# Performance work log

Measured on AMD Instinct MI355X. Metric: run time of the kernel, lower is better.

Reference implementation:

```python
import jax, jax.numpy as jnp
import numpy as np

B, S, D = 2, 1024, 1024
E, K, F, FS = 8, 2, 512, 1024

def setup_inputs() -> dict:
    key = jax.random.key(0)
    ks = jax.random.split(key, 9)
    s = lambda k, shape, fan: jax.random.normal(k, shape, jnp.float32) * (fan ** -0.5)
    return {
        "x": jax.random.normal(ks[0], (B, S, D), jnp.float32),
        "Wr": s(ks[1], (D, E), D),
        "Wg": s(ks[2], (E, D, F), D),
        "Wu": s(ks[3], (E, D, F), D),
        "Wd": s(ks[4], (E, F, D), F),
        "Sg": s(ks[5], (D, FS), D),
        "Su": s(ks[6], (D, FS), D),
        "Sd": s(ks[7], (FS, D), FS),
        "expert_bias": jnp.zeros((E,), jnp.float32),
    }

def reference(x, Wr, Wg, Wu, Wd, Sg, Su, Sd, expert_bias):
    b, s, d = x.shape
    xf = x.reshape(-1, d)                              # [T, D]
    T = xf.shape[0]
    logits = xf @ Wr + expert_bias                     # [T, E]
    top_v, top_i = jax.lax.top_k(logits, K)            # [T, K]
    probs = jax.nn.softmax(top_v, axis=-1)             # [T, K]
    # dense routing-weight matrix: zero for non-selected experts
    rw = jnp.zeros_like(logits).at[jnp.arange(T)[:, None], top_i].set(probs)  # [T, E]
    # SwiGLU experts, computed densely; routing weight zeros out unselected
    gate = jnp.einsum('td,edf->tef', xf, Wg)           # [T, E, F]
    up = jnp.einsum('td,edf->tef', xf, Wu)
    h = jax.nn.silu(gate) * up
    eo = jnp.einsum('tef,efd->ted', h, Wd)             # [T, E, D]
    out = jnp.einsum('te,ted->td', rw, eo)             # [T, D]
    # shared expert applied to all tokens
    out = out + (jax.nn.silu(xf @ Sg) * (xf @ Su)) @ Sd
    return out.reshape(b, s, d)
```

## Files before the change

kernel.cpp:

```cpp
#include <hip/hip_runtime.h>
#include <cstdint>
#include <cstddef>

typedef __attribute__((ext_vector_type(8))) short bf16x8;
typedef __attribute__((ext_vector_type(4))) float f32x4;

#define AS1 __attribute__((address_space(1)))
#define AS3 __attribute__((address_space(3)))

__device__ __forceinline__ unsigned short f2bf(float f) {
  union { float f; unsigned int u; } v; v.f = f;
  unsigned int r = v.u + 0x7fffu + ((v.u >> 16) & 1u);
  return (unsigned short)(r >> 16);
}

__device__ __forceinline__ void gll16(const unsigned short* g, unsigned short* l) {
  __builtin_amdgcn_global_load_lds((const AS1 void*)g, (AS3 void*)l, 16, 0, 0);
}


__global__ __launch_bounds__(256) void transpose_cvt_all(
    const float* __restrict__ Wg, const float* __restrict__ Wu,
    const float* __restrict__ Wd, const float* __restrict__ Sg,
    const float* __restrict__ Su, const float* __restrict__ Sd,
    const float* __restrict__ x, const float* __restrict__ Wr,
    unsigned short* __restrict__ WguT, unsigned short* __restrict__ WdT,
    unsigned short* __restrict__ SguT, unsigned short* __restrict__ SdT,
    unsigned short* __restrict__ Xb, float* __restrict__ logits) {
  const int z = blockIdx.z;
  const int tid = threadIdx.x;

  if (z == 31) {
    const int bid = blockIdx.y * 16 + blockIdx.x;
    const int wave = tid >> 6;
    const int lane = tid & 63;
#pragma unroll
    for (int it = 0; it < 2; it++) {
      const int t = bid * 8 + wave * 2 + it;
      const float* xr = x + (size_t)t * 1024;
      float acc[8];
#pragma unroll
      for (int e = 0; e < 8; e++) acc[e] = 0.f;
#pragma unroll
      for (int i = 0; i < 16; i++) {
        int d = lane + i * 64;
        float xv = xr[d];
        const float4* w = (const float4*)(Wr + d * 8);
        float4 w0 = w[0], w1 = w[1];
        acc[0] += xv * w0.x; acc[1] += xv * w0.y; acc[2] += xv * w0.z; acc[3] += xv * w0.w;
        acc[4] += xv * w1.x; acc[5] += xv * w1.y; acc[6] += xv * w1.z; acc[7] += xv * w1.w;
      }
#pragma unroll
      for (int off = 32; off > 0; off >>= 1)
#pragma unroll
        for (int e = 0; e < 8; e++) acc[e] += __shfl_down(acc[e], off);
      if (lane == 0) {
#pragma unroll
        for (int e = 0; e < 8; e++) logits[t * 8 + e] = acc[e];
      }
    }
    return;
  }

  if (z >= 27) {
    size_t off = (size_t)(z - 27) * 524288 + blockIdx.y * 32768 + blockIdx.x * 2048 + tid * 8;
    const float4* s = (const float4*)(x + off);
    float4 a = s[0], b = s[1];
    bf16x8 o = { (short)f2bf(a.x), (short)f2bf(a.y), (short)f2bf(a.z), (short)f2bf(a.w),
                 (short)f2bf(b.x), (short)f2bf(b.y), (short)f2bf(b.z), (short)f2bf(b.w) };
    *(bf16x8*)(Xb + off) = o;
    return;
  }

  const float* src; unsigned short* base; int R, C, nmul, nadd, Ksz;
  if (z < 8)       { src = Wg + (size_t)z * 524288; base = WguT + (size_t)z * 1048576; R = 1024; C = 512;  nmul = 2; nadd = 0; Ksz = 1024; }
  else if (z < 16) { src = Wu + (size_t)(z - 8) * 524288; base = WguT + (size_t)(z - 8) * 1048576; R = 1024; C = 512; nmul = 2; nadd = 1; Ksz = 1024; }
  else if (z < 24) { src = Wd + (size_t)(z - 16) * 524288; base = WdT + (size_t)(z - 16) * 524288; R = 512; C = 1024; nmul = 1; nadd = 0; Ksz = 512; }
  else if (z == 24){ src = Sg; base = SguT; R = 1024; C = 1024; nmul = 2; nadd = 0; Ksz = 1024; }
  else if (z == 25){ src = Su; base = SguT; R = 1024; C = 1024; nmul = 2; nadd = 1; Ksz = 1024; }
  else             { src = Sd; base = SdT; R = 1024; C = 1024; nmul = 1; nadd = 0; Ksz = 1024; }
  const int c0 = blockIdx.x * 64, r0 = blockIdx.y * 64;
  if (c0 >= C || r0 >= R) return;

  __shared__ float tile[64][65];
  {
    const int row = tid >> 2, cs = (tid & 3) * 16;
    const float* sp = src + (size_t)(r0 + row) * C + c0 + cs;
#pragma unroll
    for (int k = 0; k < 4; k++) {
      float4 v = ((const float4*)sp)[k];
      tile[row][cs + k * 4 + 0] = v.x; tile[row][cs + k * 4 + 1] = v.y;
      tile[row][cs + k * 4 + 2] = v.z; tile[row][cs + k * 4 + 3] = v.w;
    }
  }
  __syncthreads();
#pragma unroll
  for (int i = 0; i < 2; i++) {
    const int cc = i * 32 + (tid >> 3);
    const int rseg = (tid & 7) * 8;
    bf16x8 o;
#pragma unroll
    for (int j = 0; j < 8; j++) o[j] = (short)f2bf(tile[rseg + j][cc]);
    const int n = nmul * (c0 + cc) + nadd;
    const int k0 = r0 + rseg;
    const int p = n >> 7, r = n & 127, s = k0 >> 6;
    const int c8 = ((k0 >> 3) & 7) ^ (r & 7);
    *(bf16x8*)(base + (size_t)p * (Ksz * 128) + (size_t)s * 8192 + (r * 8 + c8) * 8) = o;
  }
}

__global__ __launch_bounds__(1024) void assign_kernel(
    const float* __restrict__ logits, const float* __restrict__ bias,
    int* __restrict__ list, int* __restrict__ ridx, float* __restrict__ rp,
    int* __restrict__ counts_g, int* __restrict__ offs_g) {
  __shared__ int cnt[8];
  __shared__ int offs[9];
  const int tid = threadIdx.x;
  if (tid < 8) cnt[tid] = 0;
  __syncthreads();
  int te[2][2], tpos[2][2];
  float tp[2][2];
#pragma unroll
  for (int it = 0; it < 2; it++) {
    int t = tid + it * 1024;
    float v[8];
#pragma unroll
    for (int e = 0; e < 8; e++) v[e] = logits[t * 8 + e] + bias[e];
    int i0 = 0;
#pragma unroll
    for (int e = 1; e < 8; e++) if (v[e] > v[i0]) i0 = e;
    int i1 = (i0 == 0) ? 1 : 0;
#pragma unroll
    for (int e = 0; e < 8; e++) if (e != i0 && v[e] > v[i1]) i1 = e;
    float pa = 1.f / (1.f + __expf(v[i1] - v[i0]));
    te[it][0] = i0; te[it][1] = i1;
    tp[it][0] = pa; tp[it][1] = 1.f - pa;
    tpos[it][0] = atomicAdd(&cnt[i0], 1);
    tpos[it][1] = atomicAdd(&cnt[i1], 1);
  }
  __syncthreads();
  if (tid == 0) {
    int s = 0;
#pragma unroll
    for (int e = 0; e < 8; e++) { offs[e] = s; s += cnt[e]; }
    offs[8] = s;
#pragma unroll
    for (int e = 0; e < 8; e++) { counts_g[e] = cnt[e]; offs_g[e] = offs[e]; }
    offs_g[8] = s;
  }
  __syncthreads();
#pragma unroll
  for (int it = 0; it < 2; it++) {
    int t = tid + it * 1024;
#pragma unroll
    for (int k = 0; k < 2; k++) {
      int grow = offs[te[it][k]] + tpos[it][k];
      list[grow] = t;
      ridx[t * 2 + k] = grow;
      rp[t * 2 + k] = tp[it][k];
    }
  }
}

#define STAGE8(b, s) \
  gll16(gA0 + (s) * 64, AsP + (b) * 8192 + wuni); \
  gll16(gA1 + (s) * 64, AsP + (b) * 8192 + 2048 + wuni); \
  gll16(gA2 + (s) * 64, AsP + (b) * 8192 + 4096 + wuni); \
  gll16(gA3 + (s) * 64, AsP + (b) * 8192 + 6144 + wuni); \
  gll16(gB + (s) * 8192, BsP + (b) * 8192 + wuni); \
  gll16(gB + (s) * 8192 + 2048, BsP + (b) * 8192 + 2048 + wuni); \
  gll16(gB + (s) * 8192 + 4096, BsP + (b) * 8192 + 4096 + wuni); \
  gll16(gB + (s) * 8192 + 6144, BsP + (b) * 8192 + 6144 + wuni);

template <int NK>
__device__ __forceinline__ void kloop64(
    const unsigned short* gA0, const unsigned short* gA1,
    const unsigned short* gA2, const unsigned short* gA3,
    const unsigned short* gB,
    unsigned short* AsP, unsigned short* BsP, const int wuni,
    const int aO0, const int aO1, const int aO2, const int aO3,
    const int bO0, const int bO1, const int bO2, const int bO3,
    const int cc0, f32x4 (&acc)[4][4]) {
  STAGE8(0, 0);
#pragma unroll
  for (int i = 0; i < NK; ++i) {
    asm volatile("s_waitcnt lgkmcnt(0)\n\ts_barrier" ::: "memory");
    if (i + 1 < NK) {
      STAGE8((i + 1) & 1, i + 1);
      asm volatile("s_waitcnt vmcnt(8)" ::: "memory");
    } else {
      asm volatile("s_waitcnt vmcnt(0)" ::: "memory");
    }
    const unsigned short* Ab = AsP + (i & 1) * 8192;
    const unsigned short* Bb = BsP + (i & 1) * 8192;
#pragma unroll
    for (int kk = 0; kk < 2; ++kk) {
      const int co = cc0 ^ (kk << 5);
      bf16x8 af[4], bf[4];
      af[0] = *(const bf16x8*)(Ab + aO0 + co);
      af[1] = *(const bf16x8*)(Ab + aO1 + co);
      af[2] = *(const bf16x8*)(Ab + aO2 + co);
      af[3] = *(const bf16x8*)(Ab + aO3 + co);
      bf[0] = *(const bf16x8*)(Bb + bO0 + co);
      bf[1] = *(const bf16x8*)(Bb + bO1 + co);
      bf[2] = *(const bf16x8*)(Bb + bO2 + co);
      bf[3] = *(const bf16x8*)(Bb + bO3 + co);
#pragma unroll
      for (int ii = 0; ii < 4; ++ii)
#pragma unroll
        for (int jj = 0; jj < 4; ++jj)
          acc[ii][jj] = __builtin_amdgcn_mfma_f32_16x16x32_bf16(af[ii], bf[jj], acc[ii][jj], 0, 0, 0);
    }
  }
}

template <int MODE>
__global__ __launch_bounds__(256, 2) void gemm_tn_kernel(
    const unsigned short* __restrict__ Xb, const unsigned short* __restrict__ He,
    const unsigned short* __restrict__ Hs, const unsigned short* __restrict__ Wgu,
    const unsigned short* __restrict__ Sgu, const unsigned short* __restrict__ Wd,
    const unsigned short* __restrict__ Sd, unsigned short* __restrict__ HeOut,
    unsigned short* __restrict__ HsOut, float* __restrict__ De, float* __restrict__ Ds,
    const int* __restrict__ list, const int* __restrict__ counts,
    const int* __restrict__ offs) {
  const int h = blockIdx.x;
  const int c = h & 7;
  const int idx = h >> 3;

  int cnt, lda, m0, n0;
  bool routed;
  const unsigned short* A;
  const unsigned short* Bt;
  const int* alist = nullptr;
  unsigned short* H = nullptr;
  float* D = nullptr;
  int ldh = 0;

  if (MODE == 0) {
    if (idx < 128) {
      routed = true;
      n0 = (idx >> 4) * 128; m0 = (idx & 15) * 128;
      cnt = counts[c]; A = Xb; alist = list + offs[c]; lda = 1024;
      Bt = Wgu + (size_t)c * 1048576 + (size_t)(n0 >> 7) * 131072;
      H = HeOut + (size_t)offs[c] * 512; ldh = 512;
    } else {
      routed = false;
      const int t2 = idx - 128;
      m0 = ((c & 1) * 8 + (t2 & 7)) * 128;
      n0 = ((c >> 1) * 4 + (t2 >> 3)) * 128;
      cnt = 2048; A = Xb; lda = 1024;
      Bt = Sgu + (size_t)(n0 >> 7) * 131072;
      H = HsOut; ldh = 1024;
    }
  } else {
    if (idx < 128) {
      routed = true;
      n0 = (idx >> 4) * 128; m0 = (idx & 15) * 128;
      cnt = counts[c]; A = He + (size_t)offs[c] * 512; lda = 512;
      Bt = Wd + (size_t)c * 524288 + (size_t)(n0 >> 7) * 65536;
      D = De + (size_t)offs[c] * 1024;
    } else {
      routed = false;
      const int t2 = idx - 128;
      m0 = ((c & 1) * 8 + (t2 & 7)) * 128;
      n0 = ((c >> 1) * 2 + (t2 >> 3)) * 128;
      cnt = 2048; A = Hs; lda = 1024;
      Bt = Sd + (size_t)(n0 >> 7) * 131072;
      D = Ds;
    }
  }
  if (m0 >= cnt) return;

  __shared__ unsigned short As[2 * 8192];
  __shared__ unsigned short Bs[2 * 8192];

  const int tid = threadIdx.x;
  const int wuni = (tid >> 6) * 512;
  const int qg = ((tid & 7) ^ ((tid >> 3) & 7)) * 8;
  const int rb = tid >> 3;

  int r0 = m0 + rb;       if (r0 >= cnt) r0 = cnt - 1;
  int r1 = m0 + 32 + rb;  if (r1 >= cnt) r1 = cnt - 1;
  int r2 = m0 + 64 + rb;  if (r2 >= cnt) r2 = cnt - 1;
  int r3 = m0 + 96 + rb;  if (r3 >= cnt) r3 = cnt - 1;
  size_t ab0, ab1, ab2, ab3;
  if (MODE == 0 && routed) {
    ab0 = (size_t)alist[r0] * lda; ab1 = (size_t)alist[r1] * lda;
    ab2 = (size_t)alist[r2] * lda; ab3 = (size_t)alist[r3] * lda;
  } else {
    ab0 = (size_t)r0 * lda; ab1 = (size_t)r1 * lda;
    ab2 = (size_t)r2 * lda; ab3 = (size_t)r3 * lda;
  }
  const unsigned short* gA0 = A + ab0 + qg;
  const unsigned short* gA1 = A + ab1 + qg;
  const unsigned short* gA2 = A + ab2 + qg;
  const unsigned short* gA3 = A + ab3 + qg;
  const unsigned short* gB = Bt + tid * 8;

  const int wave = tid >> 6;
  const int lane = tid & 63;
  const int wm = (wave & 1) * 64;
  const int wn = (wave >> 1) * 64;
  const int fl = lane & 15;
  const int q = lane >> 4;

  const int aO0 = (wm + fl) * 64, aO1 = aO0 + 1024, aO2 = aO0 + 2048, aO3 = aO0 + 3072;
  const int bO0 = (wn + fl) * 64, bO1 = bO0 + 1024, bO2 = bO0 + 2048, bO3 = bO0 + 3072;
  const int cc0 = (q ^ (fl & 7)) * 8;

  f32x4 acc[4][4];
  f32x4 zero = {0.f, 0.f, 0.f, 0.f};
#pragma unroll
  for (int i = 0; i < 4; i++)
#pragma unroll
    for (int j = 0; j < 4; j++) acc[i][j] = zero;

  if (MODE == 1 && routed)
    kloop64<8>(gA0, gA1, gA2, gA3, gB, As, Bs, wuni, aO0, aO1, aO2, aO3, bO0, bO1, bO2, bO3, cc0, acc);
  else
    kloop64<16>(gA0, gA1, gA2, gA3, gB, As, Bs, wuni, aO0, aO1, aO2, aO3, bO0, bO1, bO2, bO3, cc0, acc);

  if (MODE == 0) {
#pragma unroll
    for (int i = 0; i < 4; i++) {
#pragma unroll
      for (int j = 0; j < 4; j++) {
#pragma unroll
        for (int r = 0; r < 4; r++) {
          int grow = m0 + wm + i * 16 + q * 4 + r;
          float v = acc[i][j][r];
          float pv = __shfl_xor(v, 1);
          if ((lane & 1) == 0 && grow < cnt) {
            float s = v / (1.f + __expf(-v));
            int colh = (n0 + wn + j * 16 + fl) >> 1;
            H[(size_t)grow * ldh + colh] = f2bf(s * pv);
          }
        }
      }
    }
  } else {
#pragma unroll
    for (int i = 0; i < 4; i++) {
#pragma unroll
      for (int r = 0; r < 4; r++) {
        int grow = m0 + wm + i * 16 + q * 4 + r;
        if (grow >= cnt) continue;
#pragma unroll
        for (int j = 0; j < 4; j++) {
          int col = n0 + wn + j * 16 + fl;
          D[(size_t)grow * 1024 + col] = acc[i][j][r];
        }
      }
    }
  }
}

__global__ __launch_bounds__(256) void combine_kernel(
    const float* __restrict__ Ds, const float* __restrict__ De,
    const int* __restrict__ ridx, const float* __restrict__ rp,
    float* __restrict__ out) {
  const int t = blockIdx.x;
  const int i0 = ridx[t * 2], i1 = ridx[t * 2 + 1];
  const float p0 = rp[t * 2], p1 = rp[t * 2 + 1];
  const float4* a  = (const float4*)(Ds + (size_t)t * 1024);
  const float4* b0 = (const float4*)(De + (size_t)i0 * 1024);
  const float4* b1 = (const float4*)(De + (size_t)i1 * 1024);
  float4* o = (float4*)(out + (size_t)t * 1024);
  int c = threadIdx.x;
  float4 va = a[c], v0 = b0[c], v1 = b1[c];
  float4 r;
  r.x = va.x + p0 * v0.x + p1 * v1.x;
  r.y = va.y + p0 * v0.y + p1 * v1.y;
  r.z = va.z + p0 * v0.z + p1 * v1.z;
  r.w = va.w + p0 * v0.w + p1 * v1.w;
  o[c] = r;
}

extern "C" void kernel_launch(void* const* d_in, const int* in_sizes, int n_in,
                              void* d_out, int out_size, void* d_ws, size_t ws_size,
                              hipStream_t stream) {
  const float* x    = (const float*)d_in[0];
  const float* Wr   = (const float*)d_in[1];
  const float* Wg   = (const float*)d_in[2];
  const float* Wu   = (const float*)d_in[3];
  const float* Wd   = (const float*)d_in[4];
  const float* Sg   = (const float*)d_in[5];
  const float* Su   = (const float*)d_in[6];
  const float* Sd   = (const float*)d_in[7];
  const float* bias = (const float*)d_in[8];
  float* out = (float*)d_out;

  char* ws = (char*)d_ws;
  size_t o = 0;
  auto alloc = [&](size_t b) { char* p = ws + o; o += (b + 255) & ~(size_t)255; return p; };
  unsigned short* Xb   = (unsigned short*)alloc((size_t)2048 * 1024 * 2);
  unsigned short* WguT = (unsigned short*)alloc((size_t)8 * 1024 * 1024 * 2);
  unsigned short* WdT  = (unsigned short*)alloc((size_t)8 * 1024 * 512 * 2);
  unsigned short* SguT = (unsigned short*)alloc((size_t)2048 * 1024 * 2);
  unsigned short* SdT  = (unsigned short*)alloc((size_t)1024 * 1024 * 2);
  float* logits = (float*)alloc((size_t)2048 * 8 * 4);
  int*   list   = (int*)alloc((size_t)4096 * 4);
  int*   ridx   = (int*)alloc((size_t)2048 * 2 * 4);
  float* rp     = (float*)alloc((size_t)2048 * 2 * 4);
  int*   counts = (int*)alloc(64);
  int*   offs   = (int*)alloc(64);
  unsigned short* He = (unsigned short*)alloc((size_t)4096 * 512 * 2);
  unsigned short* Hs = (unsigned short*)alloc((size_t)2048 * 1024 * 2);
  float* De = (float*)alloc((size_t)4096 * 1024 * 4);
  float* Ds = (float*)alloc((size_t)2048 * 1024 * 4);

  transpose_cvt_all<<<dim3(16, 16, 32), 256, 0, stream>>>(Wg, Wu, Wd, Sg, Su, Sd, x, Wr,
                                                          WguT, WdT, SguT, SdT, Xb, logits);

  assign_kernel<<<1, 1024, 0, stream>>>(logits, bias, list, ridx, rp, counts, offs);

  gemm_tn_kernel<0><<<dim3(1280), 256, 0, stream>>>(
      Xb, He, Hs, WguT, SguT, WdT, SdT, He, Hs, De, Ds, list, counts, offs);
  gemm_tn_kernel<1><<<dim3(1152), 256, 0, stream>>>(
      Xb, He, Hs, WguT, SguT, WdT, SdT, He, Hs, De, Ds, list, counts, offs);

  combine_kernel<<<2048, 256, 0, stream>>>(Ds, De, ridx, rp, out);
}
```

Measured before the change: 197.1 us.

## Switch GEMM main loop to BK=32 triple-buffered LDS pipeline with three blocks per CU

The shared GEMM kernel now uses a K-tile of 32 instead of 64 and a three-stage LDS ring with two tiles prefetched ahead, in place of a double-buffered 64-wide tile. The weight pre-transpose is changed to the matching 32-wide swizzled layout. LDS per block drops, which lets launch bounds request three resident blocks per CU, and the MFMA section is wrapped in s_setprio. The aim is to hide global-load latency better and raise occupancy, at the cost of twice as many barriers and iterations per K.

```diff
diff --git a/kernel.cpp b/kernel.cpp
--- a/kernel.cpp
+++ b/kernel.cpp
@@ -103,9 +103,9 @@
     for (int j = 0; j < 8; j++) o[j] = (short)f2bf(tile[rseg + j][cc]);
     const int n = nmul * (c0 + cc) + nadd;
     const int k0 = r0 + rseg;
-    const int p = n >> 7, r = n & 127, s = k0 >> 6;
-    const int c8 = ((k0 >> 3) & 7) ^ (r & 7);
-    *(bf16x8*)(base + (size_t)p * (Ksz * 128) + (size_t)s * 8192 + (r * 8 + c8) * 8) = o;
+    const int p = n >> 7, r = n & 127, s = k0 >> 5;
+    const int c4 = ((k0 >> 3) & 3) ^ ((r >> 1) & 3);
+    *(bf16x8*)(base + (size_t)p * (Ksz * 128) + (size_t)s * 4096 + (r * 4 + c4) * 8) = o;
   }
 }
 
@@ -162,60 +162,52 @@
   }
 }
 
-#define STAGE8(b, s) \
-  gll16(gA0 + (s) * 64, AsP + (b) * 8192 + wuni); \
-  gll16(gA1 + (s) * 64, AsP + (b) * 8192 + 2048 + wuni); \
-  gll16(gA2 + (s) * 64, AsP + (b) * 8192 + 4096 + wuni); \
-  gll16(gA3 + (s) * 64, AsP + (b) * 8192 + 6144 + wuni); \
-  gll16(gB + (s) * 8192, BsP + (b) * 8192 + wuni); \
-  gll16(gB + (s) * 8192 + 2048, BsP + (b) * 8192 + 2048 + wuni); \
-  gll16(gB + (s) * 8192 + 4096, BsP + (b) * 8192 + 4096 + wuni); \
-  gll16(gB + (s) * 8192 + 6144, BsP + (b) * 8192 + 6144 + wuni);
+#define STAGE4(buf, s) { \
+  unsigned short* Ad = As + (buf) * 4096 + wuni2; \
+  unsigned short* Bd = Bs + (buf) * 4096 + wuni2; \
+  gll16(gA0 + (s) * 32, Ad); \
+  gll16(gA1 + (s) * 32, Ad + 512); \
+  gll16(gB + (s) * 4096, Bd); \
+  gll16(gB + (s) * 4096 + 512, Bd + 512); }
 
 template <int NK>
-__device__ __forceinline__ void kloop64(
+__device__ __forceinline__ void kloop32(
     const unsigned short* gA0, const unsigned short* gA1,
-    const unsigned short* gA2, const unsigned short* gA3,
     const unsigned short* gB,
-    unsigned short* AsP, unsigned short* BsP, const int wuni,
+    unsigned short* As, unsigned short* Bs, const int wuni2,
     const int aO0, const int aO1, const int aO2, const int aO3,
     const int bO0, const int bO1, const int bO2, const int bO3,
-    const int cc0, f32x4 (&acc)[4][4]) {
-  STAGE8(0, 0);
+    f32x4 (&acc)[4][4]) {
+  STAGE4(0, 0);
+  STAGE4(1, 1);
 #pragma unroll
   for (int i = 0; i < NK; ++i) {
-    asm volatile("s_waitcnt lgkmcnt(0)\n\ts_barrier" ::: "memory");
-    if (i + 1 < NK) {
-      STAGE8((i + 1) & 1, i + 1);
-      asm volatile("s_waitcnt vmcnt(8)" ::: "memory");
-    } else {
-      asm volatile("s_waitcnt vmcnt(0)" ::: "memory");
-    }
-    const unsigned short* Ab = AsP + (i & 1) * 8192;
-    const unsigned short* Bb = BsP + (i & 1) * 8192;
-#pragma unroll
-    for (int kk = 0; kk < 2; ++kk) {
-      const int co = cc0 ^ (kk << 5);
-      bf16x8 af[4], bf[4];
-      af[0] = *(const bf16x8*)(Ab + aO0 + co);
-      af[1] = *(const bf16x8*)(Ab + aO1 + co);
-      af[2] = *(const bf16x8*)(Ab + aO2 + co);
-      af[3] = *(const bf16x8*)(Ab + aO3 + co);
-      bf[0] = *(const bf16x8*)(Bb + bO0 + co);
-      bf[1] = *(const bf16x8*)(Bb + bO1 + co);
-      bf[2] = *(const bf16x8*)(Bb + bO2 + co);
-      bf[3] = *(const bf16x8*)(Bb + bO3 + co);
-#pragma unroll
-      for (int ii = 0; ii < 4; ++ii)
-#pragma unroll
-        for (int jj = 0; jj < 4; ++jj)
-          acc[ii][jj] = __builtin_amdgcn_mfma_f32_16x16x32_bf16(af[ii], bf[jj], acc[ii][jj], 0, 0, 0);
-    }
+    if (i + 1 < NK) asm volatile("s_waitcnt vmcnt(4) lgkmcnt(0)\n\ts_barrier" ::: "memory");
+    else            asm volatile("s_waitcnt vmcnt(0) lgkmcnt(0)\n\ts_barrier" ::: "memory");
+    if (i + 2 < NK) { STAGE4((i + 2) % 3, i + 2); }
+    const unsigned short* Ab = As + (i % 3) * 4096;
+    const unsigned short* Bb = Bs + (i % 3) * 4096;
+    bf16x8 af[4], bf[4];
+    af[0] = *(const bf16x8*)(Ab + aO0);
+    af[1] = *(const bf16x8*)(Ab + aO1);
+    af[2] = *(const bf16x8*)(Ab + aO2);
+    af[3] = *(const bf16x8*)(Ab + aO3);
+    bf[0] = *(const bf16x8*)(Bb + bO0);
+    bf[1] = *(const bf16x8*)(Bb + bO1);
+    bf[2] = *(const bf16x8*)(Bb + bO2);
+    bf[3] = *(const bf16x8*)(Bb + bO3);
+    __builtin_amdgcn_s_setprio(1);
+#pragma unroll
+    for (int ii = 0; ii < 4; ++ii)
+#pragma unroll
+      for (int jj = 0; jj < 4; ++jj)
+        acc[ii][jj] = __builtin_amdgcn_mfma_f32_16x16x32_bf16(af[ii], bf[jj], acc[ii][jj], 0, 0, 0);
+    __builtin_amdgcn_s_setprio(0);
   }
 }
 
 template <int MODE>
-__global__ __launch_bounds__(256, 2) void gemm_tn_kernel(
+__global__ __launch_bounds__(256, 3) void gemm_tn_kernel(
     const unsigned short* __restrict__ Xb, const unsigned short* __restrict__ He,
     const unsigned short* __restrict__ Hs, const unsigned short* __restrict__ Wgu,
     const unsigned short* __restrict__ Sgu, const unsigned short* __restrict__ Wd,
@@ -271,42 +263,38 @@
   }
   if (m0 >= cnt) return;
 
-  __shared__ unsigned short As[2 * 8192];
-  __shared__ unsigned short Bs[2 * 8192];
+  __shared__ unsigned short As[3 * 4096];
+  __shared__ unsigned short Bs[3 * 4096];
 
   const int tid = threadIdx.x;
-  const int wuni = (tid >> 6) * 512;
-  const int qg = ((tid & 7) ^ ((tid >> 3) & 7)) * 8;
-  const int rb = tid >> 3;
-
-  int r0 = m0 + rb;       if (r0 >= cnt) r0 = cnt - 1;
-  int r1 = m0 + 32 + rb;  if (r1 >= cnt) r1 = cnt - 1;
-  int r2 = m0 + 64 + rb;  if (r2 >= cnt) r2 = cnt - 1;
-  int r3 = m0 + 96 + rb;  if (r3 >= cnt) r3 = cnt - 1;
-  size_t ab0, ab1, ab2, ab3;
+  const int wave = tid >> 6;
+  const int lane = tid & 63;
+  const int wuni2 = wave * 1024;
+
+  const int achk = ((lane & 3) ^ ((lane >> 3) & 3)) * 8;
+  const int arow0 = wave * 32 + (lane >> 2);
+  const int arow1 = arow0 + 16;
+
+  int r0 = m0 + arow0; if (r0 >= cnt) r0 = cnt - 1;
+  int r1 = m0 + arow1; if (r1 >= cnt) r1 = cnt - 1;
+  size_t ab0, ab1;
   if (MODE == 0 && routed) {
     ab0 = (size_t)alist[r0] * lda; ab1 = (size_t)alist[r1] * lda;
-    ab2 = (size_t)alist[r2] * lda; ab3 = (size_t)alist[r3] * lda;
   } else {
     ab0 = (size_t)r0 * lda; ab1 = (size_t)r1 * lda;
-    ab2 = (size_t)r2 * lda; ab3 = (size_t)r3 * lda;
-  }
-  const unsigned short* gA0 = A + ab0 + qg;
-  const unsigned short* gA1 = A + ab1 + qg;
-  const unsigned short* gA2 = A + ab2 + qg;
-  const unsigned short* gA3 = A + ab3 + qg;
-  const unsigned short* gB = Bt + tid * 8;
-
-  const int wave = tid >> 6;
-  const int lane = tid & 63;
+  }
+  const unsigned short* gA0 = A + ab0 + achk;
+  const unsigned short* gA1 = A + ab1 + achk;
+  const unsigned short* gB = Bt + (wave * 128 + lane) * 8;
+
   const int wm = (wave & 1) * 64;
   const int wn = (wave >> 1) * 64;
   const int fl = lane & 15;
   const int q = lane >> 4;
 
-  const int aO0 = (wm + fl) * 64, aO1 = aO0 + 1024, aO2 = aO0 + 2048, aO3 = aO0 + 3072;
-  const int bO0 = (wn + fl) * 64, bO1 = bO0 + 1024, bO2 = bO0 + 2048, bO3 = bO0 + 3072;
-  const int cc0 = (q ^ (fl & 7)) * 8;
+  const int cr = (q ^ ((fl >> 1) & 3)) * 8;
+  const int aO0 = (wm + fl) * 32 + cr, aO1 = aO0 + 512, aO2 = aO0 + 1024, aO3 = aO0 + 1536;
+  const int bO0 = (wn + fl) * 32 + cr, bO1 = bO0 + 512, bO2 = bO0 + 1024, bO3 = bO0 + 1536;
 
   f32x4 acc[4][4];
   f32x4 zero = {0.f, 0.f, 0.f, 0.f};
@@ -316,9 +304,9 @@
     for (int j = 0; j < 4; j++) acc[i][j] = zero;
 
   if (MODE == 1 && routed)
-    kloop64<8>(gA0, gA1, gA2, gA3, gB, As, Bs, wuni, aO0, aO1, aO2, aO3, bO0, bO1, bO2, bO3, cc0, acc);
+    kloop32<16>(gA0, gA1, gB, As, Bs, wuni2, aO0, aO1, aO2, aO3, bO0, bO1, bO2, bO3, acc);
   else
-    kloop64<16>(gA0, gA1, gA2, gA3, gB, As, Bs, wuni, aO0, aO1, aO2, aO3, bO0, bO1, bO2, bO3, cc0, acc);
+    kloop32<32>(gA0, gA1, gB, As, Bs, wuni2, aO0, aO1, aO2, aO3, bO0, bO1, bO2, bO3, acc);
 
   if (MODE == 0) {
 #pragma unroll
```

Measured after the change: 195.5 us. Within noise of the previous version (-0.8%).
